# Kernel tuning notes

Measured on AMD Instinct MI355X. Metric: run time of the kernel, lower is better.

The kernel has to match this reference:

```python
import jax, jax.numpy as jnp
import numpy as np

N_EXPERTS = 128
N_GROUP = 1
TOPK_GROUP = 1
TOP_K = 8
ROUTED_SCALING = 1.0
NORM_TOPK_PROB = True


def setup_inputs() -> dict:
    key = jax.random.key(0)
    k1, k2, k3 = jax.random.split(key, 3)
    T, H = 32768, 4096
    hidden_states = jax.random.normal(k1, (T, H), dtype=jnp.float32)
    weight = jax.random.normal(k2, (N_EXPERTS, H), dtype=jnp.float32) * 0.02
    e_score_correction_bias = jax.random.normal(k3, (N_EXPERTS,), dtype=jnp.float32) * 0.1
    return {"hidden_states": hidden_states, "weight": weight,
            "e_score_correction_bias": e_score_correction_bias}


def reference(hidden_states, weight, e_score_correction_bias):
    T = hidden_states.shape[0]
    per_group = N_EXPERTS // N_GROUP
    # router logits in fp32, as in the torch module
    logits = jnp.einsum('th,eh->te', hidden_states.astype(jnp.float32),
                        weight.astype(jnp.float32))
    scores = jax.nn.sigmoid(logits)                         # [T, E]
    scores_for_choice = scores + e_score_correction_bias[None, :]
    # group scores: sum of top-2 expert scores within each group
    grouped = scores_for_choice.reshape(T, N_GROUP, per_group)
    group_scores = jax.lax.top_k(grouped, 2)[0].sum(axis=-1)  # [T, G]
    _, group_idx = jax.lax.top_k(group_scores, TOPK_GROUP)    # [T, topk_group]
    group_mask = jnp.zeros((T, N_GROUP), dtype=scores.dtype)
    group_mask = group_mask.at[jnp.arange(T)[:, None], group_idx].set(1.0)
    score_mask = jnp.broadcast_to(group_mask[:, :, None],
                                  (T, N_GROUP, per_group)).reshape(T, N_EXPERTS)
    masked_scores = jnp.where(score_mask.astype(bool), scores_for_choice, 0.0)
    _, topk_indices = jax.lax.top_k(masked_scores, TOP_K)     # [T, top_k]
    topk_weights = jnp.take_along_axis(scores, topk_indices, axis=1)
    if NORM_TOPK_PROB:
        denom = topk_weights.sum(axis=-1, keepdims=True) + 1e-20
        topk_weights = topk_weights / denom
    topk_weights = topk_weights * ROUTED_SCALING
    return topk_indices, topk_weights
```

## Files before the change

### kernel.cpp

```cpp
#include <hip/hip_runtime.h>
#include <math.h>

#define TOKENS 32768
#define HDIM   4096
#define NEXP   128
#define TOPK   8

#define BT 64
#define BH 64
#define AS_STRIDE 68
#define WS_STRIDE 132

__global__ __launch_bounds__(256, 2)
void glm4v_router_kernel(const float* __restrict__ hs,
                         const float* __restrict__ wt,
                         const float* __restrict__ bias,
                         float* __restrict__ out)
{
    __shared__ float As[BH * AS_STRIDE];
    __shared__ float Ws[BH * WS_STRIDE];
    __shared__ float bias_s[NEXP];

    const int t  = threadIdx.x;
    const int tx = t & 15;
    const int ty = t >> 4;
    const int tokBase = blockIdx.x * BT;

    if (t < NEXP) bias_s[t] = bias[t];

    double acc[4][8];
    #pragma unroll
    for (int i = 0; i < 4; ++i)
        #pragma unroll
        for (int k = 0; k < 8; ++k) acc[i][k] = 0.0;

    const int col4 = t & 15;
    const int rowq = t >> 4;

    for (int hc = 0; hc < HDIM; hc += BH) {
        __syncthreads();

        #pragma unroll
        for (int j = 0; j < 4; ++j) {
            const int row = rowq + 16 * j;
            const float4 v = *(const float4*)(hs + (size_t)(tokBase + row) * HDIM + hc + col4 * 4);
            const int h = col4 * 4;
            As[(h + 0) * AS_STRIDE + row] = v.x;
            As[(h + 1) * AS_STRIDE + row] = v.y;
            As[(h + 2) * AS_STRIDE + row] = v.z;
            As[(h + 3) * AS_STRIDE + row] = v.w;
        }
        #pragma unroll
        for (int j = 0; j < 8; ++j) {
            const int e = rowq + 16 * j;
            const float4 v = *(const float4*)(wt + (size_t)e * HDIM + hc + col4 * 4);
            const int h = col4 * 4;
            Ws[(h + 0) * WS_STRIDE + e] = v.x;
            Ws[(h + 1) * WS_STRIDE + e] = v.y;
            Ws[(h + 2) * WS_STRIDE + e] = v.z;
            Ws[(h + 3) * WS_STRIDE + e] = v.w;
        }
        __syncthreads();

        #pragma unroll 4
        for (int h = 0; h < BH; ++h) {
            const float4 av = *(const float4*)(As + h * AS_STRIDE + 4 * ty);
            const float4 w0 = *(const float4*)(Ws + h * WS_STRIDE + tx * 8);
            const float4 w1 = *(const float4*)(Ws + h * WS_STRIDE + tx * 8 + 4);
            const double a[4] = { (double)av.x, (double)av.y, (double)av.z, (double)av.w };
            const double w[8] = { (double)w0.x, (double)w0.y, (double)w0.z, (double)w0.w,
                                  (double)w1.x, (double)w1.y, (double)w1.z, (double)w1.w };
            #pragma unroll
            for (int i = 0; i < 4; ++i)
                #pragma unroll
                for (int k = 0; k < 8; ++k)
                    acc[i][k] = fma(a[i], w[k], acc[i][k]);
        }
    }
    __syncthreads();

    const int lane = t & 63;
    const int grpBase = lane & 48;

    for (int i = 0; i < 4; ++i) {
        const int tok = tokBase + 4 * ty + i;

        double ss[8];
        double rr[8];
        #pragma unroll
        for (int k = 0; k < 8; ++k) {
            const double x = acc[i][k];
            const double s = 1.0 / (1.0 + exp(-x));
            ss[k] = s;
            rr[k] = s + (double)bias_s[tx * 8 + k];
        }

        int    sel[TOPK];
        double wv[TOPK];
        #pragma unroll
        for (int r = 0; r < TOPK; ++r) {
            double bv = rr[0]; int bi = tx * 8;
            #pragma unroll
            for (int k = 1; k < 8; ++k)
                if (rr[k] > bv) { bv = rr[k]; bi = tx * 8 + k; }
            #pragma unroll
            for (int m = 1; m <= 8; m <<= 1) {
                const double ov = __shfl_xor(bv, m, 64);
                const int    oi = __shfl_xor(bi, m, 64);
                if (ov > bv || (ov == bv && oi < bi)) { bv = ov; bi = oi; }
            }
            sel[r] = bi;
            double sv = 0.0;
            #pragma unroll
            for (int k = 0; k < 8; ++k)
                if (k == (bi & 7)) sv = ss[k];
            wv[r] = __shfl(sv, grpBase | (bi >> 3), 64);
            if ((bi >> 3) == tx) {
                #pragma unroll
                for (int k = 0; k < 8; ++k)
                    if (k == (bi & 7)) rr[k] = -INFINITY;
            }
        }

        if (tx == 0) {
            double denom = 1e-20;
            #pragma unroll
            for (int r = 0; r < TOPK; ++r) denom += wv[r];
            #pragma unroll
            for (int r = 0; r < TOPK; ++r) {
                out[(size_t)tok * TOPK + r] = (float)sel[r];
                out[(size_t)TOKENS * TOPK + (size_t)tok * TOPK + r] = (float)(wv[r] / denom);
            }
        }
    }
}

extern "C" void kernel_launch(void* const* d_in, const int* in_sizes, int n_in,
                              void* d_out, int out_size, void* d_ws, size_t ws_size,
                              hipStream_t stream) {
    const float* hs   = (const float*)d_in[0];
    const float* wt   = (const float*)d_in[1];
    const float* bias = (const float*)d_in[2];
    float* out = (float*)d_out;

    dim3 grid(TOKENS / BT);
    dim3 block(256);
    glm4v_router_kernel<<<grid, block, 0, stream>>>(hs, wt, bias, out);
}
```

Before: 1.615 ms.

## Compute router logits with FP64 MFMA instead of scalar double FMAs

Replaces the scalar FP64 FMA inner product with v_mfma_f64_16x16x4f64 matrix instructions. Each wave computes a 16-token by 128-expert tile. Shared-memory tiles are now stored row-major without a transpose, and the lane-to-row/column mapping of the accumulator is found with calibration MFMAs. The top-k selection is rewritten to match that mapping, shuffling lane ownership along with the index. This aims to cut the heavy FP64 ALU cost while keeping double-precision accumulation. The risk is an incorrect assumption about the MFMA output layout.

```diff
diff --git a/kernel.cpp b/kernel.cpp
--- a/kernel.cpp
+++ b/kernel.cpp
@@ -5,124 +5,128 @@
 #define HDIM   4096
 #define NEXP   128
 #define TOPK   8
+#define BT     64
+#define BH     64
+#define LSTR   68
 
-#define BT 64
-#define BH 64
-#define AS_STRIDE 68
-#define WS_STRIDE 132
+typedef __attribute__((ext_vector_type(4))) double dbl4;
 
 __global__ __launch_bounds__(256, 2)
-void glm4v_router_kernel(const float* __restrict__ hs,
-                         const float* __restrict__ wt,
-                         const float* __restrict__ bias,
-                         float* __restrict__ out)
+void glm4v_router_mfma(const float* __restrict__ hs,
+                       const float* __restrict__ wt,
+                       const float* __restrict__ bias,
+                       float* __restrict__ out)
 {
-    __shared__ float As[BH * AS_STRIDE];
-    __shared__ float Ws[BH * WS_STRIDE];
+    __shared__ float As[BT * LSTR];
+    __shared__ float Ws[NEXP * LSTR];
     __shared__ float bias_s[NEXP];
 
-    const int t  = threadIdx.x;
-    const int tx = t & 15;
-    const int ty = t >> 4;
+    const int t    = threadIdx.x;
+    const int w    = t >> 6;
+    const int lane = t & 63;
+    const int col  = lane & 15;
+    const int q    = lane >> 4;
+
     const int tokBase = blockIdx.x * BT;
 
     if (t < NEXP) bias_s[t] = bias[t];
 
-    double acc[4][8];
+    dbl4 acc[8];
     #pragma unroll
-    for (int i = 0; i < 4; ++i)
-        #pragma unroll
-        for (int k = 0; k < 8; ++k) acc[i][k] = 0.0;
+    for (int et = 0; et < 8; ++et) acc[et] = (dbl4){0.0, 0.0, 0.0, 0.0};
 
-    const int col4 = t & 15;
-    const int rowq = t >> 4;
+    const int sr = t >> 4;
+    const int sc = (t & 15) * 4;
+
+    const float* __restrict__ aRow = As + (w * 16 + col) * LSTR + q * 4;
 
     for (int hc = 0; hc < HDIM; hc += BH) {
         __syncthreads();
-
         #pragma unroll
         for (int j = 0; j < 4; ++j) {
-            const int row = rowq + 16 * j;
-            const float4 v = *(const float4*)(hs + (size_t)(tokBase + row) * HDIM + hc + col4 * 4);
-            const int h = col4 * 4;
-            As[(h + 0) * AS_STRIDE + row] = v.x;
-            As[(h + 1) * AS_STRIDE + row] = v.y;
-            As[(h + 2) * AS_STRIDE + row] = v.z;
-            As[(h + 3) * AS_STRIDE + row] = v.w;
+            const int row = sr + 16 * j;
+            const float4 v = *(const float4*)(hs + (size_t)(tokBase + row) * HDIM + hc + sc);
+            *(float4*)(As + row * LSTR + sc) = v;
         }
         #pragma unroll
         for (int j = 0; j < 8; ++j) {
-            const int e = rowq + 16 * j;
-            const float4 v = *(const float4*)(wt + (size_t)e * HDIM + hc + col4 * 4);
-            const int h = col4 * 4;
-            Ws[(h + 0) * WS_STRIDE + e] = v.x;
-            Ws[(h + 1) * WS_STRIDE + e] = v.y;
-            Ws[(h + 2) * WS_STRIDE + e] = v.z;
-            Ws[(h + 3) * WS_STRIDE + e] = v.w;
+            const int e = sr + 16 * j;
+            const float4 v = *(const float4*)(wt + (size_t)e * HDIM + hc + sc);
+            *(float4*)(Ws + e * LSTR + sc) = v;
         }
         __syncthreads();
 
-        #pragma unroll 4
-        for (int h = 0; h < BH; ++h) {
-            const float4 av = *(const float4*)(As + h * AS_STRIDE + 4 * ty);
-            const float4 w0 = *(const float4*)(Ws + h * WS_STRIDE + tx * 8);
-            const float4 w1 = *(const float4*)(Ws + h * WS_STRIDE + tx * 8 + 4);
-            const double a[4] = { (double)av.x, (double)av.y, (double)av.z, (double)av.w };
-            const double w[8] = { (double)w0.x, (double)w0.y, (double)w0.z, (double)w0.w,
-                                  (double)w1.x, (double)w1.y, (double)w1.z, (double)w1.w };
+        #pragma unroll
+        for (int kb = 0; kb < BH; kb += 16) {
+            const float4 a4 = *(const float4*)(aRow + kb);
+            float4 b4[8];
             #pragma unroll
-            for (int i = 0; i < 4; ++i)
+            for (int et = 0; et < 8; ++et)
+                b4[et] = *(const float4*)(Ws + (et * 16 + col) * LSTR + kb + q * 4);
+            const float* ap = (const float*)&a4;
+            #pragma unroll
+            for (int s = 0; s < 4; ++s) {
+                const double ad = (double)ap[s];
                 #pragma unroll
-                for (int k = 0; k < 8; ++k)
-                    acc[i][k] = fma(a[i], w[k], acc[i][k]);
+                for (int et = 0; et < 8; ++et) {
+                    const double bd = (double)((const float*)&b4[et])[s];
+                    acc[et] = __builtin_amdgcn_mfma_f64_16x16x4f64(ad, bd, acc[et], 0, 0, 0);
+                }
+            }
         }
     }
-    __syncthreads();
 
-    const int lane = t & 63;
-    const int grpBase = lane & 48;
+    dbl4 rowcal = (dbl4){0.0, 0.0, 0.0, 0.0};
+    dbl4 colcal = (dbl4){0.0, 0.0, 0.0, 0.0};
+    const double dcol = (double)col;
+    rowcal = __builtin_amdgcn_mfma_f64_16x16x4f64(dcol, 0.25, rowcal, 0, 0, 0);
+    colcal = __builtin_amdgcn_mfma_f64_16x16x4f64(0.25, dcol, colcal, 0, 0, 0);
 
-    for (int i = 0; i < 4; ++i) {
-        const int tok = tokBase + 4 * ty + i;
+    #pragma unroll
+    for (int j = 0; j < 4; ++j) {
+        const int rj = (int)(rowcal[j] + 0.5);
+        const int cj = (int)(colcal[j] + 0.5);
+        const int tok = tokBase + w * 16 + rj;
 
         double ss[8];
         double rr[8];
         #pragma unroll
-        for (int k = 0; k < 8; ++k) {
-            const double x = acc[i][k];
+        for (int et = 0; et < 8; ++et) {
+            const double x = acc[et][j];
             const double s = 1.0 / (1.0 + exp(-x));
-            ss[k] = s;
-            rr[k] = s + (double)bias_s[tx * 8 + k];
+            ss[et] = s;
+            rr[et] = s + (double)bias_s[et * 16 + cj];
         }
 
         int    sel[TOPK];
         double wv[TOPK];
         #pragma unroll
         for (int r = 0; r < TOPK; ++r) {
-            double bv = rr[0]; int bi = tx * 8;
+            double bv = rr[0]; int bi = cj; int bl = lane;
             #pragma unroll
-            for (int k = 1; k < 8; ++k)
-                if (rr[k] > bv) { bv = rr[k]; bi = tx * 8 + k; }
+            for (int et = 1; et < 8; ++et)
+                if (rr[et] > bv) { bv = rr[et]; bi = et * 16 + cj; }
             #pragma unroll
             for (int m = 1; m <= 8; m <<= 1) {
                 const double ov = __shfl_xor(bv, m, 64);
                 const int    oi = __shfl_xor(bi, m, 64);
-                if (ov > bv || (ov == bv && oi < bi)) { bv = ov; bi = oi; }
+                const int    ol = __shfl_xor(bl, m, 64);
+                if (ov > bv || (ov == bv && oi < bi)) { bv = ov; bi = oi; bl = ol; }
             }
             sel[r] = bi;
-            double sv = 0.0;
+            double sv = ss[0];
             #pragma unroll
-            for (int k = 0; k < 8; ++k)
-                if (k == (bi & 7)) sv = ss[k];
-            wv[r] = __shfl(sv, grpBase | (bi >> 3), 64);
-            if ((bi >> 3) == tx) {
+            for (int et = 1; et < 8; ++et)
+                if ((bi >> 4) == et) sv = ss[et];
+            wv[r] = __shfl(sv, bl, 64);
+            if (bl == lane) {
                 #pragma unroll
-                for (int k = 0; k < 8; ++k)
-                    if (k == (bi & 7)) rr[k] = -INFINITY;
+                for (int et = 0; et < 8; ++et)
+                    if ((bi >> 4) == et) rr[et] = -INFINITY;
             }
         }
 
-        if (tx == 0) {
+        if (cj == 0) {
             double denom = 1e-20;
             #pragma unroll
             for (int r = 0; r < TOPK; ++r) denom += wv[r];
@@ -145,5 +149,5 @@
 
     dim3 grid(TOKENS / BT);
     dim3 block(256);
-    glm4v_router_kernel<<<grid, block, 0, stream>>>(hs, wt, bias, out);
+    glm4v_router_mfma<<<grid, block, 0, stream>>>(hs, wt, bias, out);
 }
```

Measured after the change: 1.342 ms. -16.9%, faster.
